# Optimization experiments

Measured on AMD Instinct MI355X. Metric: run time of the kernel, lower is better.

## Reference

```python
import jax, jax.numpy as jnp
import numpy as np

DIM = 1024
NUM_HEADS = 16
HEAD_DIM = DIM // NUM_HEADS
SCALE = HEAD_DIM ** (-0.5)
B, N = 2, 2048


def setup_inputs() -> dict:
    key = jax.random.key(0)
    ks = jax.random.split(key, 9)
    s = DIM ** (-0.5)
    return {
        "x": jax.random.normal(ks[0], (B, N, DIM), dtype=jnp.float32),
        "Wq": jax.random.normal(ks[1], (DIM, DIM), dtype=jnp.float32) * s,
        "bq": jax.random.normal(ks[2], (DIM,), dtype=jnp.float32) * 0.01,
        "Wk": jax.random.normal(ks[3], (DIM, DIM), dtype=jnp.float32) * s,
        "bk": jax.random.normal(ks[4], (DIM,), dtype=jnp.float32) * 0.01,
        "Wv": jax.random.normal(ks[5], (DIM, DIM), dtype=jnp.float32) * s,
        "bv": jax.random.normal(ks[6], (DIM,), dtype=jnp.float32) * 0.01,
        "Wp": jax.random.normal(ks[7], (DIM, DIM), dtype=jnp.float32) * s,
        "bp": jax.random.normal(ks[8], (DIM,), dtype=jnp.float32) * 0.01,
    }


def reference(x, Wq, bq, Wk, bk, Wv, bv, Wp, bp):
    Bb, Nn, C = x.shape
    # Linear layers (torch Linear: x @ W.T + b)
    q = x @ Wq.T + bq
    k = x @ Wk.T + bk
    v = x @ Wv.T + bv
    # [B, H, N, Dh]
    q = q.reshape(Bb, Nn, NUM_HEADS, HEAD_DIM).transpose(0, 2, 1, 3) * SCALE
    k = k.reshape(Bb, Nn, NUM_HEADS, HEAD_DIM).transpose(0, 2, 1, 3)
    v = v.reshape(Bb, Nn, NUM_HEADS, HEAD_DIM).transpose(0, 2, 1, 3)
    # float32 scores (original casts q,k to float before matmul)
    attn = jnp.einsum("bhnd,bhmd->bhnm", q.astype(jnp.float32), k.astype(jnp.float32))
    attn = jax.nn.softmax(attn, axis=-1).astype(x.dtype)
    out = jnp.einsum("bhnm,bhmd->bhnd", attn, v)
    out = out.transpose(0, 2, 1, 3).reshape(Bb, Nn, C)
    return out @ Wp.T + bp
```

## Files before the change

### kernel.cpp

```cpp
#include <hip/hip_runtime.h>
#include <hip/hip_bf16.h>
#include <stdint.h>

#define SEQ   2048
#define NDIM  1024
#define NH    16
#define DH    64
#define NB    2
#define MROWS (NB*SEQ)
#define ATTN_SCALE 0.125f

typedef __attribute__((ext_vector_type(8))) short bf16x8;
typedef __attribute__((ext_vector_type(4))) float f32x4;


__device__ __forceinline__ unsigned short f2bf(float f) {
  union { float f; unsigned int u; } v; v.f = f;
  unsigned int u = v.u;
  return (unsigned short)((u + 0x7fffu + ((u >> 16) & 1u)) >> 16);
}

__device__ __forceinline__ void gld16(const void* g, void* l) {
  __builtin_amdgcn_global_load_lds(
      (const __attribute__((address_space(1))) void*)g,
      (__attribute__((address_space(3))) void*)l,
      16, 0, 0);
}

__global__ __launch_bounds__(256) void cvt_all(
    const float* __restrict__ x,  const float* __restrict__ wq,
    const float* __restrict__ wk, const float* __restrict__ wv,
    const float* __restrict__ wp,
    unsigned short* __restrict__ xb,  unsigned short* __restrict__ wqb,
    unsigned short* __restrict__ wkb, unsigned short* __restrict__ wvb,
    unsigned short* __restrict__ wpb)
{
  int c = blockIdx.x * 256 + threadIdx.x;
  const float* s; unsigned short* d;
  if (c < (MROWS*NDIM/8)) { s = x; d = xb; }
  else {
    c -= MROWS*NDIM/8;
    int w = c >> 17; c &= (1<<17)-1;
    s = (w==0)?wq:(w==1)?wk:(w==2)?wv:wp;
    d = (w==0)?wqb:(w==1)?wkb:(w==2)?wvb:wpb;
  }
  size_t off = (size_t)c * 8;
  const float4* sp = (const float4*)(s + off);
  float4 a = sp[0], b4 = sp[1];
  unsigned int u0 = (unsigned)f2bf(a.x)  | ((unsigned)f2bf(a.y)  << 16);
  unsigned int u1 = (unsigned)f2bf(a.z)  | ((unsigned)f2bf(a.w)  << 16);
  unsigned int u2 = (unsigned)f2bf(b4.x) | ((unsigned)f2bf(b4.y) << 16);
  unsigned int u3 = (unsigned)f2bf(b4.z) | ((unsigned)f2bf(b4.w) << 16);
  uint4 o; o.x = u0; o.y = u1; o.z = u2; o.w = u3;
  *(uint4*)(d + off) = o;
}

__device__ __forceinline__ void gemm128_loop(
    const unsigned short* __restrict__ A0,
    const unsigned short* __restrict__ B0,
    int K, f32x4 acc[4][4], char* ldsA, char* ldsB)
{
  const int tid = threadIdx.x;
  const int lane = tid & 63;
  const int g    = lane >> 4;
  const int l15  = lane & 15;
  const int wv   = tid >> 6;
  const int wm   = wv >> 1;
  const int wn   = wv & 1;

  int srow[2], scol[2];
#pragma unroll
  for (int p = 0; p < 2; ++p) {
    int idx = p*256 + tid;
    int row = idx >> 2, cpos = idx & 3;
    srow[p] = row;
    scol[p] = (cpos ^ ((row >> 1) & 3)) * 8;
  }
  int offA[4], offB[4];
#pragma unroll
  for (int f = 0; f < 4; ++f) {
    int ra = wm*64 + f*16 + l15;
    offA[f] = ra*64 + ((g ^ ((ra >> 1) & 3)) * 16);
    int rb = wn*64 + f*16 + l15;
    offB[f] = rb*64 + ((g ^ ((rb >> 1) & 3)) * 16);
  }

  for (int k0 = 0; k0 < K; k0 += 32) {
#pragma unroll
    for (int p = 0; p < 2; ++p) {
      gld16(A0 + (size_t)srow[p]*K + k0 + scol[p], ldsA + p*4096 + wv*1024);
      gld16(B0 + (size_t)srow[p]*K + k0 + scol[p], ldsB + p*4096 + wv*1024);
    }
    __syncthreads();
    bf16x8 af[4], bfr[4];
#pragma unroll
    for (int f = 0; f < 4; ++f) {
      af[f]  = *(const bf16x8*)(ldsA + offA[f]);
      bfr[f] = *(const bf16x8*)(ldsB + offB[f]);
    }
#pragma unroll
    for (int i = 0; i < 4; ++i)
#pragma unroll
      for (int j = 0; j < 4; ++j)
        acc[i][j] = __builtin_amdgcn_mfma_f32_16x16x32_bf16(af[i], bfr[j], acc[i][j], 0, 0, 0);
    __syncthreads();
  }
}

__global__ __launch_bounds__(256, 3) void gemm_qkv(
    const unsigned short* __restrict__ xb,
    const unsigned short* __restrict__ wqb, const unsigned short* __restrict__ wkb,
    const unsigned short* __restrict__ wvb,
    const float* __restrict__ bq, const float* __restrict__ bk, const float* __restrict__ bv,
    unsigned short* __restrict__ qb, unsigned short* __restrict__ kb,
    unsigned short* __restrict__ vtb)
{
  __shared__ __align__(16) char lds[16384];
  const int z = blockIdx.z;
  const unsigned short* W = (z==0)?wqb:(z==1)?wkb:wvb;
  const float* bias = (z==0)?bq:(z==1)?bk:bv;
  const int n0 = blockIdx.x * 128, m0 = blockIdx.y * 128;

  f32x4 acc[4][4];
#pragma unroll
  for (int i = 0; i < 4; ++i)
#pragma unroll
    for (int j = 0; j < 4; ++j) acc[i][j] = (f32x4){0.f, 0.f, 0.f, 0.f};

  gemm128_loop(xb + (size_t)m0*NDIM, W + (size_t)n0*NDIM, NDIM, acc, lds, lds + 8192);

  const int lane = threadIdx.x & 63, g = lane >> 4, l15 = lane & 15;
  const int wvx = threadIdx.x >> 6, wm = wvx >> 1, wn = wvx & 1;

  if (z < 2) {
    unsigned short* out = (z==0) ? qb : kb;
#pragma unroll
    for (int i = 0; i < 4; ++i)
#pragma unroll
      for (int j = 0; j < 4; ++j) {
        int col = n0 + wn*64 + j*16 + l15;
        float bb = bias[col];
#pragma unroll
        for (int r = 0; r < 4; ++r) {
          int row = m0 + wm*64 + i*16 + g*4 + r;
          out[(size_t)row*NDIM + col] = f2bf(acc[i][j][r] + bb);
        }
      }
  } else {
#pragma unroll
    for (int i = 0; i < 4; ++i)
#pragma unroll
      for (int j = 0; j < 4; ++j) {
        int col = n0 + wn*64 + j*16 + l15;
        float bb = bias[col];
        int row0 = m0 + wm*64 + i*16 + g*4;
        int b_ = row0 >> 11, n_ = row0 & (SEQ-1);
        unsigned long long pk =
            (unsigned long long)f2bf(acc[i][j][0] + bb)
          | ((unsigned long long)f2bf(acc[i][j][1] + bb) << 16)
          | ((unsigned long long)f2bf(acc[i][j][2] + bb) << 32)
          | ((unsigned long long)f2bf(acc[i][j][3] + bb) << 48);
        *(unsigned long long*)(vtb + ((size_t)(b_*NDIM + col))*SEQ + n_) = pk;
      }
  }
}

__global__ __launch_bounds__(256, 2) void attn_fwd(
    const unsigned short* __restrict__ qb, const unsigned short* __restrict__ kb,
    const unsigned short* __restrict__ vtb, unsigned short* __restrict__ ob)
{
  __shared__ __align__(16) char lds[32768];
  char* Ks = lds;
  char* Vs = lds + 8192;
  const int tid = threadIdx.x, lane = tid & 63, g = lane >> 4, l15 = lane & 15;
  const int wvx = tid >> 6;
  char* Pw = lds + 16384 + wvx*4096;
  const int bh = blockIdx.y, b_ = bh >> 4, h = bh & 15;
  const int qbase = blockIdx.x*128 + wvx*32;

  bf16x8 qf[2][2];
#pragma unroll
  for (int fn = 0; fn < 2; ++fn)
#pragma unroll
    for (int kc = 0; kc < 2; ++kc) {
      size_t row = (size_t)(b_*SEQ + qbase + fn*16 + l15);
      qf[fn][kc] = *(const bf16x8*)(qb + row*NDIM + h*DH + kc*32 + g*8);
    }

  float m_[2] = {-3.0e38f, -3.0e38f};
  float l_[2] = {0.f, 0.f};
  f32x4 o_[2][4];
#pragma unroll
  for (int fn = 0; fn < 2; ++fn)
#pragma unroll
    for (int fd = 0; fd < 4; ++fd) o_[fn][fd] = (f32x4){0.f, 0.f, 0.f, 0.f};

  for (int t = 0; t < SEQ/64; ++t) {
    const int k0t = t*64;
#pragma unroll
    for (int p = 0; p < 2; ++p) {
      int idx = p*256 + tid;
      int row = idx >> 3, cpos = idx & 7;
      int gc8 = (cpos ^ (row & 7)) * 8;
      gld16(kb  + ((size_t)(b_*SEQ + k0t + row))*NDIM + h*DH + gc8,
            Ks + p*4096 + wvx*1024);
      gld16(vtb + ((size_t)(b_*NDIM + h*DH + row))*SEQ + k0t + gc8,
            Vs + p*4096 + wvx*1024);
    }
    __syncthreads();

    bf16x8 kf[4][2];
#pragma unroll
    for (int fm = 0; fm < 4; ++fm)
#pragma unroll
      for (int kc = 0; kc < 2; ++kc) {
        int row = fm*16 + l15;
        kf[fm][kc] = *(const bf16x8*)(Ks + row*128 + (((kc*4+g) ^ (row & 7))*16));
      }

    f32x4 st[2][4];
#pragma unroll
    for (int fn = 0; fn < 2; ++fn)
#pragma unroll
      for (int fm = 0; fm < 4; ++fm) st[fn][fm] = (f32x4){0.f, 0.f, 0.f, 0.f};
#pragma unroll
    for (int kc = 0; kc < 2; ++kc)
#pragma unroll
      for (int fn = 0; fn < 2; ++fn)
#pragma unroll
        for (int fm = 0; fm < 4; ++fm)
          st[fn][fm] = __builtin_amdgcn_mfma_f32_16x16x32_bf16(kf[fm][kc], qf[fn][kc], st[fn][fm], 0, 0, 0);

#pragma unroll
    for (int fn = 0; fn < 2; ++fn) {
      float xs[4][4];
      float tmax = -3.0e38f;
#pragma unroll
      for (int fm = 0; fm < 4; ++fm)
#pragma unroll
        for (int r = 0; r < 4; ++r) {
          float v = st[fn][fm][r] * ATTN_SCALE;
          xs[fm][r] = v;
          tmax = fmaxf(tmax, v);
        }
      tmax = fmaxf(tmax, __shfl_xor(tmax, 16));
      tmax = fmaxf(tmax, __shfl_xor(tmax, 32));
      float mnew  = fmaxf(m_[fn], tmax);
      float alpha = __expf(m_[fn] - mnew);
      m_[fn] = mnew;
      float rsum = 0.f;
      const int prow = fn*16 + l15;
#pragma unroll
      for (int fm = 0; fm < 4; ++fm) {
        float p0 = __expf(xs[fm][0] - mnew);
        float p1 = __expf(xs[fm][1] - mnew);
        float p2 = __expf(xs[fm][2] - mnew);
        float p3 = __expf(xs[fm][3] - mnew);
        rsum += (p0 + p1) + (p2 + p3);
        unsigned long long pk =
            (unsigned long long)f2bf(p0)
          | ((unsigned long long)f2bf(p1) << 16)
          | ((unsigned long long)f2bf(p2) << 32)
          | ((unsigned long long)f2bf(p3) << 48);
        *(unsigned long long*)(Pw + prow*128 + (((fm*2 + (g>>1)) ^ (prow & 7))*16) + (g & 1)*8) = pk;
      }
      rsum += __shfl_xor(rsum, 16);
      rsum += __shfl_xor(rsum, 32);
      l_[fn] = l_[fn]*alpha + rsum;
#pragma unroll
      for (int fd = 0; fd < 4; ++fd)
#pragma unroll
        for (int r = 0; r < 4; ++r) o_[fn][fd][r] *= alpha;
    }

    bf16x8 vf[4][2];
#pragma unroll
    for (int fd = 0; fd < 4; ++fd)
#pragma unroll
      for (int ks = 0; ks < 2; ++ks) {
        int row = fd*16 + l15;
        vf[fd][ks] = *(const bf16x8*)(Vs + row*128 + (((ks*4+g) ^ (row & 7))*16));
      }
    bf16x8 pf[2][2];
#pragma unroll
    for (int fn = 0; fn < 2; ++fn)
#pragma unroll
      for (int ks = 0; ks < 2; ++ks) {
        int row = fn*16 + l15;
        pf[fn][ks] = *(const bf16x8*)(Pw + row*128 + (((ks*4+g) ^ (row & 7))*16));
      }
#pragma unroll
    for (int ks = 0; ks < 2; ++ks)
#pragma unroll
      for (int fn = 0; fn < 2; ++fn)
#pragma unroll
        for (int fd = 0; fd < 4; ++fd)
          o_[fn][fd] = __builtin_amdgcn_mfma_f32_16x16x32_bf16(vf[fd][ks], pf[fn][ks], o_[fn][fd], 0, 0, 0);

    __syncthreads();
  }

#pragma unroll
  for (int fn = 0; fn < 2; ++fn) {
    float inv = 1.f / l_[fn];
    size_t row = (size_t)(b_*SEQ + qbase + fn*16 + l15);
#pragma unroll
    for (int fd = 0; fd < 4; ++fd) {
      unsigned long long pk =
          (unsigned long long)f2bf(o_[fn][fd][0]*inv)
        | ((unsigned long long)f2bf(o_[fn][fd][1]*inv) << 16)
        | ((unsigned long long)f2bf(o_[fn][fd][2]*inv) << 32)
        | ((unsigned long long)f2bf(o_[fn][fd][3]*inv) << 48);
      *(unsigned long long*)(ob + row*NDIM + h*DH + fd*16 + g*4) = pk;
    }
  }
}

__global__ __launch_bounds__(256, 3) void gemm_proj(
    const unsigned short* __restrict__ ob, const unsigned short* __restrict__ wpb,
    const float* __restrict__ bp, float* __restrict__ out)
{
  __shared__ __align__(16) char lds[16384];
  const int n0 = blockIdx.x * 128, m0 = blockIdx.y * 128;
  f32x4 acc[4][4];
#pragma unroll
  for (int i = 0; i < 4; ++i)
#pragma unroll
    for (int j = 0; j < 4; ++j) acc[i][j] = (f32x4){0.f, 0.f, 0.f, 0.f};

  gemm128_loop(ob + (size_t)m0*NDIM, wpb + (size_t)n0*NDIM, NDIM, acc, lds, lds + 8192);

  const int lane = threadIdx.x & 63, g = lane >> 4, l15 = lane & 15;
  const int wvx = threadIdx.x >> 6, wm = wvx >> 1, wn = wvx & 1;
#pragma unroll
  for (int i = 0; i < 4; ++i)
#pragma unroll
    for (int j = 0; j < 4; ++j) {
      int col = n0 + wn*64 + j*16 + l15;
      float bb = bp[col];
#pragma unroll
      for (int r = 0; r < 4; ++r) {
        int row = m0 + wm*64 + i*16 + g*4 + r;
        out[(size_t)row*NDIM + col] = acc[i][j][r] + bb;
      }
    }
}

extern "C" void kernel_launch(void* const* d_in, const int* in_sizes, int n_in,
                              void* d_out, int out_size, void* d_ws, size_t ws_size,
                              hipStream_t stream) {
  const float* x  = (const float*)d_in[0];
  const float* Wq = (const float*)d_in[1];
  const float* bq = (const float*)d_in[2];
  const float* Wk = (const float*)d_in[3];
  const float* bk = (const float*)d_in[4];
  const float* Wv = (const float*)d_in[5];
  const float* bv = (const float*)d_in[6];
  const float* Wp = (const float*)d_in[7];
  const float* bp = (const float*)d_in[8];
  float* out = (float*)d_out;

  char* ws = (char*)d_ws;
  const size_t MB = (size_t)1 << 20;
  unsigned short* xb  = (unsigned short*)(ws + 0*MB);
  unsigned short* wqb = (unsigned short*)(ws + 8*MB);
  unsigned short* wkb = (unsigned short*)(ws + 10*MB);
  unsigned short* wvb = (unsigned short*)(ws + 12*MB);
  unsigned short* wpb = (unsigned short*)(ws + 14*MB);
  unsigned short* qb  = (unsigned short*)(ws + 16*MB);
  unsigned short* kb  = (unsigned short*)(ws + 24*MB);
  unsigned short* vtb = (unsigned short*)(ws + 32*MB);
  unsigned short* ob  = (unsigned short*)(ws + 40*MB);

  hipLaunchKernelGGL(cvt_all, dim3(4096), dim3(256), 0, stream,
                     x, Wq, Wk, Wv, Wp, xb, wqb, wkb, wvb, wpb);
  hipLaunchKernelGGL(gemm_qkv, dim3(NDIM/128, MROWS/128, 3), dim3(256), 0, stream,
                     xb, wqb, wkb, wvb, bq, bk, bv, qb, kb, vtb);
  hipLaunchKernelGGL(attn_fwd, dim3(SEQ/128, NB*NH), dim3(256), 0, stream,
                     qb, kb, vtb, ob);
  hipLaunchKernelGGL(gemm_proj, dim3(NDIM/128, MROWS/128), dim3(256), 0, stream,
                     ob, wpb, bp, out);
}
```

Baseline: 216.0 us.

## Double-buffer attention K/V, use exp2 softmax with folded scale, widen GEMM K-tile

The attention kernel now prefetches the next K/V tile into a second LDS buffer while the current one is computed. The softmax scale and log2(e) are folded into Q in the QKV epilogue, so the loop uses exp2 directly. Output rescaling is skipped when no lane's max grows, and the row-sum reduction is deferred to the end. The GEMM loop moves to a K-step of 64 with a new swizzle, and the projection GEMM uses 64-row tiles to get more blocks. These changes cost extra LDS and an explicit vmcnt drain each step, and may lower occupancy.

```diff
diff --git a/kernel.cpp b/kernel.cpp
--- a/kernel.cpp
+++ b/kernel.cpp
@@ -8,7 +8,7 @@
 #define DH    64
 #define NB    2
 #define MROWS (NB*SEQ)
-#define ATTN_SCALE 0.125f
+#define S2SCALE (0.125f * 1.44269504f)
 
 typedef __attribute__((ext_vector_type(8))) short bf16x8;
 typedef __attribute__((ext_vector_type(4))) float f32x4;
@@ -18,6 +18,19 @@
   union { float f; unsigned int u; } v; v.f = f;
   unsigned int u = v.u;
   return (unsigned short)((u + 0x7fffu + ((u >> 16) & 1u)) >> 16);
+}
+
+__device__ __forceinline__ float exp2fast(float x) {
+#if __has_builtin(__builtin_amdgcn_exp2f)
+  return __builtin_amdgcn_exp2f(x);
+#else
+  float r; asm volatile("v_exp_f32 %0, %1" : "=v"(r) : "v"(x)); return r;
+#endif
+}
+
+__device__ __forceinline__ void drain_vmem() {
+  asm volatile("s_waitcnt vmcnt(0)" ::: "memory");
+  __builtin_amdgcn_sched_barrier(0);
 }
 
 __device__ __forceinline__ void gld16(const void* g, void* l) {
@@ -55,54 +68,74 @@
   *(uint4*)(d + off) = o;
 }
 
-__device__ __forceinline__ void gemm128_loop(
+template<int BM>
+__device__ __forceinline__ void gemm_loop(
     const unsigned short* __restrict__ A0,
     const unsigned short* __restrict__ B0,
-    int K, f32x4 acc[4][4], char* ldsA, char* ldsB)
+    int K, f32x4 (&acc)[BM/32][4], char* ldsA, char* ldsB)
 {
+  constexpr int MI   = BM/32;
+  constexpr int APIT = BM/32;
   const int tid = threadIdx.x;
-  const int lane = tid & 63;
-  const int g    = lane >> 4;
-  const int l15  = lane & 15;
-  const int wv   = tid >> 6;
-  const int wm   = wv >> 1;
-  const int wn   = wv & 1;
-
-  int srow[2], scol[2];
-#pragma unroll
-  for (int p = 0; p < 2; ++p) {
+  const int lane = tid & 63, g = lane >> 4, l15 = lane & 15;
+  const int wv = tid >> 6, wm = wv >> 1, wn = wv & 1;
+
+  int srowA[APIT], scolA[APIT], srowB[4], scolB[4];
+#pragma unroll
+  for (int p = 0; p < APIT; ++p) {
     int idx = p*256 + tid;
-    int row = idx >> 2, cpos = idx & 3;
-    srow[p] = row;
-    scol[p] = (cpos ^ ((row >> 1) & 3)) * 8;
-  }
-  int offA[4], offB[4];
+    int row = idx >> 3, c = idx & 7;
+    srowA[p] = row;
+    scolA[p] = (c ^ (row & 7)) * 8;
+  }
+#pragma unroll
+  for (int p = 0; p < 4; ++p) {
+    int idx = p*256 + tid;
+    int row = idx >> 3, c = idx & 7;
+    srowB[p] = row;
+    scolB[p] = (c ^ (row & 7)) * 8;
+  }
+  int offA[MI][2], offB[4][2];
+#pragma unroll
+  for (int f = 0; f < MI; ++f) {
+    int ra = wm*(BM/2) + f*16 + l15;
+#pragma unroll
+    for (int kc = 0; kc < 2; ++kc)
+      offA[f][kc] = ra*128 + (((kc*4 + g) ^ (ra & 7)) * 16);
+  }
 #pragma unroll
   for (int f = 0; f < 4; ++f) {
-    int ra = wm*64 + f*16 + l15;
-    offA[f] = ra*64 + ((g ^ ((ra >> 1) & 3)) * 16);
     int rb = wn*64 + f*16 + l15;
-    offB[f] = rb*64 + ((g ^ ((rb >> 1) & 3)) * 16);
-  }
-
-  for (int k0 = 0; k0 < K; k0 += 32) {
-#pragma unroll
-    for (int p = 0; p < 2; ++p) {
-      gld16(A0 + (size_t)srow[p]*K + k0 + scol[p], ldsA + p*4096 + wv*1024);
-      gld16(B0 + (size_t)srow[p]*K + k0 + scol[p], ldsB + p*4096 + wv*1024);
-    }
+#pragma unroll
+    for (int kc = 0; kc < 2; ++kc)
+      offB[f][kc] = rb*128 + (((kc*4 + g) ^ (rb & 7)) * 16);
+  }
+
+  for (int k0 = 0; k0 < K; k0 += 64) {
+#pragma unroll
+    for (int p = 0; p < APIT; ++p)
+      gld16(A0 + (size_t)srowA[p]*K + k0 + scolA[p], ldsA + p*4096 + wv*1024);
+#pragma unroll
+    for (int p = 0; p < 4; ++p)
+      gld16(B0 + (size_t)srowB[p]*K + k0 + scolB[p], ldsB + p*4096 + wv*1024);
+    drain_vmem();
     __syncthreads();
-    bf16x8 af[4], bfr[4];
-#pragma unroll
-    for (int f = 0; f < 4; ++f) {
-      af[f]  = *(const bf16x8*)(ldsA + offA[f]);
-      bfr[f] = *(const bf16x8*)(ldsB + offB[f]);
-    }
-#pragma unroll
-    for (int i = 0; i < 4; ++i)
-#pragma unroll
-      for (int j = 0; j < 4; ++j)
-        acc[i][j] = __builtin_amdgcn_mfma_f32_16x16x32_bf16(af[i], bfr[j], acc[i][j], 0, 0, 0);
+    bf16x8 af[MI][2], bfr[4][2];
+#pragma unroll
+    for (int f = 0; f < MI; ++f)
+#pragma unroll
+      for (int kc = 0; kc < 2; ++kc) af[f][kc] = *(const bf16x8*)(ldsA + offA[f][kc]);
+#pragma unroll
+    for (int f = 0; f < 4; ++f)
+#pragma unroll
+      for (int kc = 0; kc < 2; ++kc) bfr[f][kc] = *(const bf16x8*)(ldsB + offB[f][kc]);
+#pragma unroll
+    for (int kc = 0; kc < 2; ++kc)
+#pragma unroll
+      for (int i = 0; i < MI; ++i)
+#pragma unroll
+        for (int j = 0; j < 4; ++j)
+          acc[i][j] = __builtin_amdgcn_mfma_f32_16x16x32_bf16(af[i][kc], bfr[j][kc], acc[i][j], 0, 0, 0);
     __syncthreads();
   }
 }
@@ -115,7 +148,7 @@
     unsigned short* __restrict__ qb, unsigned short* __restrict__ kb,
     unsigned short* __restrict__ vtb)
 {
-  __shared__ __align__(16) char lds[16384];
+  __shared__ __align__(16) char lds[32768];
   const int z = blockIdx.z;
   const unsigned short* W = (z==0)?wqb:(z==1)?wkb:wvb;
   const float* bias = (z==0)?bq:(z==1)?bk:bv;
@@ -127,13 +160,14 @@
 #pragma unroll
     for (int j = 0; j < 4; ++j) acc[i][j] = (f32x4){0.f, 0.f, 0.f, 0.f};
 
-  gemm128_loop(xb + (size_t)m0*NDIM, W + (size_t)n0*NDIM, NDIM, acc, lds, lds + 8192);
+  gemm_loop<128>(xb + (size_t)m0*NDIM, W + (size_t)n0*NDIM, NDIM, acc, lds, lds + 16384);
 
   const int lane = threadIdx.x & 63, g = lane >> 4, l15 = lane & 15;
   const int wvx = threadIdx.x >> 6, wm = wvx >> 1, wn = wvx & 1;
 
   if (z < 2) {
     unsigned short* out = (z==0) ? qb : kb;
+    const float sc = (z==0) ? S2SCALE : 1.0f;
 #pragma unroll
     for (int i = 0; i < 4; ++i)
 #pragma unroll
@@ -143,7 +177,7 @@
 #pragma unroll
         for (int r = 0; r < 4; ++r) {
           int row = m0 + wm*64 + i*16 + g*4 + r;
-          out[(size_t)row*NDIM + col] = f2bf(acc[i][j][r] + bb);
+          out[(size_t)row*NDIM + col] = f2bf((acc[i][j][r] + bb) * sc);
         }
       }
   } else {
@@ -169,45 +203,64 @@
     const unsigned short* __restrict__ qb, const unsigned short* __restrict__ kb,
     const unsigned short* __restrict__ vtb, unsigned short* __restrict__ ob)
 {
-  __shared__ __align__(16) char lds[32768];
-  char* Ks = lds;
-  char* Vs = lds + 8192;
+  __shared__ __align__(16) char lds[49152];
   const int tid = threadIdx.x, lane = tid & 63, g = lane >> 4, l15 = lane & 15;
   const int wvx = tid >> 6;
-  char* Pw = lds + 16384 + wvx*4096;
+  char* Pw = lds + 32768 + wvx*4096;
   const int bh = blockIdx.y, b_ = bh >> 4, h = bh & 15;
   const int qbase = blockIdx.x*128 + wvx*32;
 
+  int srow[2], scol[2];
+#pragma unroll
+  for (int p = 0; p < 2; ++p) {
+    int idx = p*256 + tid;
+    int row = idx >> 3, c = idx & 7;
+    srow[p] = row;
+    scol[p] = (c ^ (row & 7)) * 8;
+  }
+
   bf16x8 qf[2][2];
 #pragma unroll
+  for (int fn = 0; fn < 2; ++fn) {
+    size_t row = (size_t)(b_*SEQ + qbase + fn*16 + l15);
+#pragma unroll
+    for (int kc = 0; kc < 2; ++kc)
+      qf[fn][kc] = *(const bf16x8*)(qb + row*NDIM + h*DH + kc*32 + g*8);
+  }
+
+  float m2[2]   = {-3.0e38f, -3.0e38f};
+  float lacc[2] = {0.f, 0.f};
+  f32x4 o_[2][4];
+#pragma unroll
   for (int fn = 0; fn < 2; ++fn)
 #pragma unroll
-    for (int kc = 0; kc < 2; ++kc) {
-      size_t row = (size_t)(b_*SEQ + qbase + fn*16 + l15);
-      qf[fn][kc] = *(const bf16x8*)(qb + row*NDIM + h*DH + kc*32 + g*8);
+    for (int fd = 0; fd < 4; ++fd) o_[fn][fd] = (f32x4){0.f, 0.f, 0.f, 0.f};
+
+#pragma unroll
+  for (int p = 0; p < 2; ++p) {
+    gld16(kb  + ((size_t)(b_*SEQ + srow[p]))*NDIM + h*DH + scol[p],
+          lds + p*4096 + wvx*1024);
+    gld16(vtb + ((size_t)(b_*NDIM + h*DH + srow[p]))*SEQ + scol[p],
+          lds + 8192 + p*4096 + wvx*1024);
+  }
+  drain_vmem();
+  __syncthreads();
+
+  int cur = 0;
+  for (int t = 0; t < SEQ/64; ++t) {
+    if (t < SEQ/64 - 1) {
+      const int k0n = (t+1)*64;
+      char* Kd = lds + (cur^1)*16384;
+#pragma unroll
+      for (int p = 0; p < 2; ++p) {
+        gld16(kb  + ((size_t)(b_*SEQ + k0n + srow[p]))*NDIM + h*DH + scol[p],
+              Kd + p*4096 + wvx*1024);
+        gld16(vtb + ((size_t)(b_*NDIM + h*DH + srow[p]))*SEQ + k0n + scol[p],
+              Kd + 8192 + p*4096 + wvx*1024);
+      }
     }
-
-  float m_[2] = {-3.0e38f, -3.0e38f};
-  float l_[2] = {0.f, 0.f};
-  f32x4 o_[2][4];
-#pragma unroll
-  for (int fn = 0; fn < 2; ++fn)
-#pragma unroll
-    for (int fd = 0; fd < 4; ++fd) o_[fn][fd] = (f32x4){0.f, 0.f, 0.f, 0.f};
-
-  for (int t = 0; t < SEQ/64; ++t) {
-    const int k0t = t*64;
-#pragma unroll
-    for (int p = 0; p < 2; ++p) {
-      int idx = p*256 + tid;
-      int row = idx >> 3, cpos = idx & 7;
-      int gc8 = (cpos ^ (row & 7)) * 8;
-      gld16(kb  + ((size_t)(b_*SEQ + k0t + row))*NDIM + h*DH + gc8,
-            Ks + p*4096 + wvx*1024);
-      gld16(vtb + ((size_t)(b_*NDIM + h*DH + row))*SEQ + k0t + gc8,
-            Vs + p*4096 + wvx*1024);
-    }
-    __syncthreads();
+    char* Ks = lds + cur*16384;
+    char* Vs = Ks + 8192;
 
     bf16x8 kf[4][2];
 #pragma unroll
@@ -233,30 +286,32 @@
 
 #pragma unroll
     for (int fn = 0; fn < 2; ++fn) {
-      float xs[4][4];
       float tmax = -3.0e38f;
 #pragma unroll
       for (int fm = 0; fm < 4; ++fm)
 #pragma unroll
-        for (int r = 0; r < 4; ++r) {
-          float v = st[fn][fm][r] * ATTN_SCALE;
-          xs[fm][r] = v;
-          tmax = fmaxf(tmax, v);
-        }
+        for (int r = 0; r < 4; ++r)
+          tmax = fmaxf(tmax, st[fn][fm][r]);
       tmax = fmaxf(tmax, __shfl_xor(tmax, 16));
       tmax = fmaxf(tmax, __shfl_xor(tmax, 32));
-      float mnew  = fmaxf(m_[fn], tmax);
-      float alpha = __expf(m_[fn] - mnew);
-      m_[fn] = mnew;
-      float rsum = 0.f;
+      if (__any(tmax > m2[fn])) {
+        float mnew  = fmaxf(m2[fn], tmax);
+        float alpha = exp2fast(m2[fn] - mnew);
+        m2[fn] = mnew;
+        lacc[fn] *= alpha;
+#pragma unroll
+        for (int fd = 0; fd < 4; ++fd)
+#pragma unroll
+          for (int r = 0; r < 4; ++r) o_[fn][fd][r] *= alpha;
+      }
       const int prow = fn*16 + l15;
 #pragma unroll
       for (int fm = 0; fm < 4; ++fm) {
-        float p0 = __expf(xs[fm][0] - mnew);
-        float p1 = __expf(xs[fm][1] - mnew);
-        float p2 = __expf(xs[fm][2] - mnew);
-        float p3 = __expf(xs[fm][3] - mnew);
-        rsum += (p0 + p1) + (p2 + p3);
+        float p0 = exp2fast(st[fn][fm][0] - m2[fn]);
+        float p1 = exp2fast(st[fn][fm][1] - m2[fn]);
+        float p2 = exp2fast(st[fn][fm][2] - m2[fn]);
+        float p3 = exp2fast(st[fn][fm][3] - m2[fn]);
+        lacc[fn] += (p0 + p1) + (p2 + p3);
         unsigned long long pk =
             (unsigned long long)f2bf(p0)
           | ((unsigned long long)f2bf(p1) << 16)
@@ -264,13 +319,6 @@
           | ((unsigned long long)f2bf(p3) << 48);
         *(unsigned long long*)(Pw + prow*128 + (((fm*2 + (g>>1)) ^ (prow & 7))*16) + (g & 1)*8) = pk;
       }
-      rsum += __shfl_xor(rsum, 16);
-      rsum += __shfl_xor(rsum, 32);
-      l_[fn] = l_[fn]*alpha + rsum;
-#pragma unroll
-      for (int fd = 0; fd < 4; ++fd)
-#pragma unroll
-        for (int r = 0; r < 4; ++r) o_[fn][fd][r] *= alpha;
     }
 
     bf16x8 vf[4][2];
@@ -297,12 +345,17 @@
         for (int fd = 0; fd < 4; ++fd)
           o_[fn][fd] = __builtin_amdgcn_mfma_f32_16x16x32_bf16(vf[fd][ks], pf[fn][ks], o_[fn][fd], 0, 0, 0);
 
+    drain_vmem();
     __syncthreads();
+    cur ^= 1;
   }
 
 #pragma unroll
   for (int fn = 0; fn < 2; ++fn) {
-    float inv = 1.f / l_[fn];
+    float l = lacc[fn];
+    l += __shfl_xor(l, 16);
+    l += __shfl_xor(l, 32);
+    float inv = 1.f / l;
     size_t row = (size_t)(b_*SEQ + qbase + fn*16 + l15);
 #pragma unroll
     for (int fd = 0; fd < 4; ++fd) {
@@ -316,31 +369,31 @@
   }
 }
 
-__global__ __launch_bounds__(256, 3) void gemm_proj(
+__global__ __launch_bounds__(256, 2) void gemm_proj(
     const unsigned short* __restrict__ ob, const unsigned short* __restrict__ wpb,
     const float* __restrict__ bp, float* __restrict__ out)
 {
-  __shared__ __align__(16) char lds[16384];
-  const int n0 = blockIdx.x * 128, m0 = blockIdx.y * 128;
-  f32x4 acc[4][4];
-#pragma unroll
-  for (int i = 0; i < 4; ++i)
+  __shared__ __align__(16) char lds[24576];
+  const int n0 = blockIdx.x * 128, m0 = blockIdx.y * 64;
+  f32x4 acc[2][4];
+#pragma unroll
+  for (int i = 0; i < 2; ++i)
 #pragma unroll
     for (int j = 0; j < 4; ++j) acc[i][j] = (f32x4){0.f, 0.f, 0.f, 0.f};
 
-  gemm128_loop(ob + (size_t)m0*NDIM, wpb + (size_t)n0*NDIM, NDIM, acc, lds, lds + 8192);
+  gemm_loop<64>(ob + (size_t)m0*NDIM, wpb + (size_t)n0*NDIM, NDIM, acc, lds, lds + 8192);
 
   const int lane = threadIdx.x & 63, g = lane >> 4, l15 = lane & 15;
   const int wvx = threadIdx.x >> 6, wm = wvx >> 1, wn = wvx & 1;
 #pragma unroll
-  for (int i = 0; i < 4; ++i)
+  for (int i = 0; i < 2; ++i)
 #pragma unroll
     for (int j = 0; j < 4; ++j) {
       int col = n0 + wn*64 + j*16 + l15;
       float bb = bp[col];
 #pragma unroll
       for (int r = 0; r < 4; ++r) {
-        int row = m0 + wm*64 + i*16 + g*4 + r;
+        int row = m0 + wm*32 + i*16 + g*4 + r;
         out[(size_t)row*NDIM + col] = acc[i][j][r] + bb;
       }
     }
@@ -378,6 +431,6 @@
                      xb, wqb, wkb, wvb, bq, bk, bv, qb, kb, vtb);
   hipLaunchKernelGGL(attn_fwd, dim3(SEQ/128, NB*NH), dim3(256), 0, stream,
                      qb, kb, vtb, ob);
-  hipLaunchKernelGGL(gemm_proj, dim3(NDIM/128, MROWS/128), dim3(256), 0, stream,
+  hipLaunchKernelGGL(gemm_proj, dim3(NDIM/128, MROWS/64), dim3(256), 0, stream,
                      ob, wpb, bp, out);
 }
```

Result: faster. 198.6 us (-8.0%).
